# Kernel optimization log

Hardware: AMD Instinct MI355X
Metric: run time of the kernel (lower is better)

Reference implementation:

```python
import jax, jax.numpy as jnp
import numpy as np

THRESH = 0.5
MARGIN = 0.1
SCALE_POS = 2.0
SCALE_NEG = 40.0
EPS = 1e-5


def setup_inputs() -> dict:
    key = jax.random.key(0)
    k1, k2 = jax.random.split(key)
    B, D, C = 8192, 512, 512
    feats = jax.random.normal(k1, (B, D), dtype=jnp.float32)
    labels = jax.random.randint(k2, (B,), 0, C, dtype=jnp.int32)
    return {"feats": feats, "labels": labels}


def reference(feats, labels):
    B = feats.shape[0]
    inv_b = 1.0 / B
    # L2-normalize rows, cosine similarity matrix [B, B]
    f = feats / jnp.linalg.norm(feats, axis=1, keepdims=True)
    sim = f @ f.T

    same = labels[:, None] == labels[None, :]
    # positive pairs: same label AND sim < 1 - eps (excludes self-similarity)
    pos_mask = same & (sim < 1.0 - EPS)
    neg_mask = ~same

    pos_cnt = jnp.sum(pos_mask, axis=1)
    neg_cnt = jnp.sum(neg_mask, axis=1)
    valid1 = (pos_cnt >= 1) & (neg_cnt >= 1)  # row contributes to avg_ap/avg_an

    pos_sum_sim = jnp.sum(jnp.where(pos_mask, sim, 0.0), axis=1)
    neg_sum_sim = jnp.sum(jnp.where(neg_mask, sim, 0.0), axis=1)
    mean_pos = pos_sum_sim / jnp.maximum(pos_cnt, 1)
    mean_neg = neg_sum_sim / jnp.maximum(neg_cnt, 1)

    min_pos = jnp.min(jnp.where(pos_mask, sim, jnp.inf), axis=1)
    max_neg = jnp.max(jnp.where(neg_mask, sim, -jnp.inf), axis=1)

    # hard mining: neg_pair + margin > min(pos), pos_pair - margin < max(neg)
    neg_sel = neg_mask & (sim + MARGIN > min_pos[:, None])
    pos_sel = pos_mask & (sim - MARGIN < max_neg[:, None])
    valid2 = (jnp.sum(pos_sel, axis=1) >= 1) & (jnp.sum(neg_sel, axis=1) >= 1)
    valid = valid1 & valid2

    pos_exp = jnp.sum(jnp.where(pos_sel, jnp.exp(-SCALE_POS * (sim - THRESH)), 0.0), axis=1)
    neg_exp = jnp.sum(jnp.where(neg_sel, jnp.exp(SCALE_NEG * (sim - THRESH)), 0.0), axis=1)
    row_loss = (1.0 / SCALE_POS) * jnp.log1p(pos_exp) + (1.0 / SCALE_NEG) * jnp.log1p(neg_exp)

    loss = jnp.sum(jnp.where(valid, row_loss, 0.0)) * inv_b
    avg_ap = jnp.sum(jnp.where(valid1, mean_pos, 0.0)) * inv_b
    avg_an = jnp.sum(jnp.where(valid1, mean_neg, 0.0)) * inv_b
    return (loss.reshape(-1), avg_ap, avg_an)
```

## Files before the change

### kernel.cpp

```cpp
#include <hip/hip_runtime.h>
#include <math.h>

typedef float floatx4 __attribute__((ext_vector_type(4)));
typedef short short8 __attribute__((ext_vector_type(8)));
typedef unsigned short ushort4v __attribute__((ext_vector_type(4)));
typedef unsigned short ushort8v __attribute__((ext_vector_type(8)));

#define MARGIN_ 0.1f
#define THRESH_ 0.5f

__device__ __forceinline__ unsigned short f2bf(float f){
  unsigned int x = __float_as_uint(f);
  x += 0x7FFFu + ((x >> 16) & 1u);
  return (unsigned short)(x >> 16);
}
__device__ __forceinline__ float bf2f(unsigned short u){
  return __uint_as_float(((unsigned int)u) << 16);
}

__device__ __forceinline__ void gld16(const unsigned short* g, unsigned short* l){
  __builtin_amdgcn_global_load_lds(
      (const __attribute__((address_space(1))) unsigned int*)(g),
      (__attribute__((address_space(3))) unsigned int*)(l), 16, 0, 0);
}

__global__ __launch_bounds__(64) void k_norm(const float* __restrict__ feats,
                                             unsigned short* __restrict__ fbf){
  const int row = blockIdx.x;
  const int l = threadIdx.x;
  const float* rp = feats + (size_t)row * 512;
  float4 v0 = ((const float4*)rp)[2 * l];
  float4 v1 = ((const float4*)rp)[2 * l + 1];
  float ss = v0.x*v0.x + v0.y*v0.y + v0.z*v0.z + v0.w*v0.w
           + v1.x*v1.x + v1.y*v1.y + v1.z*v1.z + v1.w*v1.w;
  #pragma unroll
  for(int m = 1; m < 64; m <<= 1) ss += __shfl_xor(ss, m);
  const float rn = 1.0f / sqrtf(ss);
  short8 pk;
  pk[0] = (short)f2bf(v0.x*rn); pk[1] = (short)f2bf(v0.y*rn);
  pk[2] = (short)f2bf(v0.z*rn); pk[3] = (short)f2bf(v0.w*rn);
  pk[4] = (short)f2bf(v1.x*rn); pk[5] = (short)f2bf(v1.y*rn);
  pk[6] = (short)f2bf(v1.z*rn); pk[7] = (short)f2bf(v1.w*rn);
  ((short8*)(fbf + (size_t)row * 512))[l] = pk;
}

__global__ __launch_bounds__(256) void k_hist(const int* __restrict__ labels, int Bn,
                                              int* __restrict__ cnt){
  __shared__ int h[512];
  for(int i = threadIdx.x; i < 512; i += 256) h[i] = 0;
  __syncthreads();
  for(int i = threadIdx.x; i < Bn; i += 256) atomicAdd(&h[labels[i]], 1);
  __syncthreads();
  for(int i = threadIdx.x; i < 512; i += 256) cnt[i] = h[i];
}

__global__ __launch_bounds__(256) void k_perm(const int* __restrict__ labels,
                                              unsigned short* __restrict__ labp, int Bn){
  const int i = blockIdx.x * 256 + threadIdx.x;
  if(i < Bn) labp[i] = (unsigned short)labels[(i & ~63) + ((i & 3) * 16) + ((i >> 2) & 15)];
}

__global__ __launch_bounds__(256) void k_gemm_sym(const unsigned short* __restrict__ fbf,
                                                  unsigned short* __restrict__ simb,
                                                  int Bn){
  const int bx = blockIdx.x, by = blockIdx.y;
  if(by > bx) return;
  const bool diag = (by == bx);

  __shared__ __align__(16) unsigned short Ald[128 * 32];
  __shared__ __align__(16) unsigned short Bld[128 * 32];

  const int t = threadIdx.x;
  const int lane = t & 63, wave = t >> 6;
  const int wm = wave >> 1, wn = wave & 1;
  const int lc = lane & 15, lk = lane >> 4;
  const int row0 = by * 128, col0 = bx * 128;

  floatx4 acc[4][4];
  #pragma unroll
  for(int i = 0; i < 4; i++)
    #pragma unroll
    for(int j = 0; j < 4; j++) acc[i][j] = (floatx4){0.f, 0.f, 0.f, 0.f};

  const int rsub  = lane >> 2;
  const int slotg = (lane & 3) ^ ((lane >> 3) & 3);
  const unsigned short* gA0 = fbf + (size_t)(row0 + wave*32 + rsub) * 512 + slotg * 8;
  const unsigned short* gB0 = fbf + (size_t)(col0 + wave*32 + rsub) * 512 + slotg * 8;
  unsigned short* lA0 = Ald + wave * 1024;
  unsigned short* lB0 = Bld + wave * 1024;
  const int kswz = lk ^ ((lc >> 1) & 3);

  for(int k0 = 0; k0 < 512; k0 += 32){
    __syncthreads();
    gld16(gA0 + k0,            lA0);
    gld16(gA0 + 16*512 + k0,   lA0 + 512);
    gld16(gB0 + k0,            lB0);
    gld16(gB0 + 16*512 + k0,   lB0 + 512);
    __syncthreads();
    short8 av[4], bv[4];
    #pragma unroll
    for(int mi = 0; mi < 4; mi++) av[mi] = ((const short8*)Ald)[(wm*64 + mi*16 + lc)*4 + kswz];
    #pragma unroll
    for(int ni = 0; ni < 4; ni++) bv[ni] = ((const short8*)Bld)[(wn*64 + ni*16 + lc)*4 + kswz];
    #pragma unroll
    for(int mi = 0; mi < 4; mi++)
      #pragma unroll
      for(int ni = 0; ni < 4; ni++)
        acc[mi][ni] = __builtin_amdgcn_mfma_f32_16x16x32_bf16(av[mi], bv[ni], acc[mi][ni], 0, 0, 0);
  }

  unsigned short b[4][4][4];
  #pragma unroll
  for(int mi = 0; mi < 4; mi++)
    #pragma unroll
    for(int ni = 0; ni < 4; ni++)
      #pragma unroll
      for(int r = 0; r < 4; r++) b[mi][ni][r] = f2bf(acc[mi][ni][r]);

  #pragma unroll
  for(int mi = 0; mi < 4; mi++){
    #pragma unroll
    for(int r = 0; r < 4; r++){
      const int row = row0 + wm*64 + mi*16 + lk*4 + r;
      ushort4v v;
      v[0] = b[mi][0][r]; v[1] = b[mi][1][r]; v[2] = b[mi][2][r]; v[3] = b[mi][3][r];
      *(ushort4v*)(simb + (size_t)row * Bn + col0 + wn*64 + lc*4) = v;
    }
  }

  if(!diag){
    #pragma unroll
    for(int ni = 0; ni < 4; ni++){
      const size_t crow = (size_t)(col0 + wn*64 + ni*16 + lc) * Bn;
      #pragma unroll
      for(int r = 0; r < 4; r++){
        ushort4v v;
        v[0] = b[0][ni][r]; v[1] = b[1][ni][r]; v[2] = b[2][ni][r]; v[3] = b[3][ni][r];
        *(ushort4v*)(simb + crow + row0 + wm*64 + 16*lk + 4*r) = v;
      }
    }
  }
}

template<int NPT>
__global__ __launch_bounds__(256) void k_fused(const unsigned short* __restrict__ simb,
                                               const int* __restrict__ labels,
                                               const unsigned short* __restrict__ labp,
                                               const int* __restrict__ cnt,
                                               float* __restrict__ rl,
                                               float* __restrict__ apv,
                                               float* __restrict__ anv, int Bn){
  const int row = blockIdx.x;
  const int t = threadIdx.x, lane = t & 63, wave = t >> 6;
  const unsigned short* srow = simb + (size_t)row * Bn;
  const int labi = labels[row];
  const int a = row & 63;
  const int selfpos = (row & ~63) + ((a & 15) * 4) + (a >> 4);

  __shared__ float rq0[4], rq1[4], rq2[4], rq3[4];
  __shared__ int fl[2];
  if(t < 2) fl[t] = 0;

  ushort8v sv[NPT];
  unsigned int pmask[NPT], nmask[NPT];

  float ps = 0.f, tot = 0.f, mn = INFINITY, mx = -INFINITY;
  #pragma unroll
  for(int c = 0; c < NPT; c++){
    const int idx = c * 256 + t;
    sv[c] = ((const ushort8v*)srow)[idx];
    const ushort8v lb = ((const ushort8v*)labp)[idx];
    const int j0 = idx * 8;
    const unsigned int selfm =
        ((unsigned int)(selfpos - j0) < 8u) ? (1u << (selfpos - j0)) : 0u;
    unsigned int sm = 0;
    #pragma unroll
    for(int e = 0; e < 8; e++) sm |= (((int)lb[e] == labi) ? 1u : 0u) << e;
    const unsigned int pm = sm & ~selfm;
    pmask[c] = pm;
    nmask[c] = (~sm) & 0xFFu;
    #pragma unroll
    for(int e = 0; e < 8; e++){
      const float s = bf2f(sv[c][e]);
      tot += s;
      const bool p = (pm >> e) & 1u;
      const bool n = (nmask[c] >> e) & 1u;
      ps += p ? s : 0.f;
      mn = p ? fminf(mn, s) : mn;
      mx = n ? fmaxf(mx, s) : mx;
    }
    if(selfm) tot -= bf2f(sv[c][selfpos - j0]);
  }
  #pragma unroll
  for(int m = 1; m < 64; m <<= 1){
    ps += __shfl_xor(ps, m); tot += __shfl_xor(tot, m);
    mn = fminf(mn, __shfl_xor(mn, m)); mx = fmaxf(mx, __shfl_xor(mx, m));
  }
  if(lane == 0){ rq0[wave] = ps; rq1[wave] = tot; rq2[wave] = mn; rq3[wave] = mx; }
  __syncthreads();
  const float bps    = rq0[0] + rq0[1] + rq0[2] + rq0[3];
  const float btot   = rq1[0] + rq1[1] + rq1[2] + rq1[3];
  const float minpos = fminf(fminf(rq2[0], rq2[1]), fminf(rq2[2], rq2[3]));
  const float maxneg = fmaxf(fmaxf(rq3[0], rq3[1]), fmaxf(rq3[2], rq3[3]));
  __syncthreads();

  float pe = 0.f, ne = 0.f;
  bool pA = false, nA = false;
  #pragma unroll
  for(int c = 0; c < NPT; c++){
    #pragma unroll
    for(int e = 0; e < 8; e++){
      const float s = bf2f(sv[c][e]);
      const bool psel = ((pmask[c] >> e) & 1u) && (s - MARGIN_ < maxneg);
      const bool nsel = ((nmask[c] >> e) & 1u) && (s + MARGIN_ > minpos);
      const float arg = psel ? (THRESH_ - s) * 2.0f : (s - THRESH_) * 40.0f;
      const float ex = __expf(arg);
      pe += psel ? ex : 0.f;
      ne += nsel ? ex : 0.f;
      pA = pA || psel;
      nA = nA || nsel;
    }
  }
  const unsigned long long bp = __ballot((int)pA);
  const unsigned long long bn = __ballot((int)nA);
  #pragma unroll
  for(int m = 1; m < 64; m <<= 1){
    pe += __shfl_xor(pe, m); ne += __shfl_xor(ne, m);
  }
  if(lane == 0){
    rq0[wave] = pe; rq1[wave] = ne;
    if(bp) fl[0] = 1;
    if(bn) fl[1] = 1;
  }
  __syncthreads();
  if(t == 0){
    const float spe = rq0[0] + rq0[1] + rq0[2] + rq0[3];
    const float sne = rq1[0] + rq1[1] + rq1[2] + rq1[3];
    const int c = cnt[labi];
    const float pc = (float)(c - 1);
    const float nc = (float)(Bn - c);
    const bool v1 = (pc >= 1.f) && (nc >= 1.f);
    const bool valid = v1 && (fl[0] != 0) && (fl[1] != 0);
    rl[row]  = valid ? (0.5f * log1pf(spe) + 0.025f * log1pf(sne)) : 0.f;
    apv[row] = v1 ? bps / fmaxf(pc, 1.f) : 0.f;
    anv[row] = v1 ? (btot - bps) / fmaxf(nc, 1.f) : 0.f;
  }
}

__global__ __launch_bounds__(256) void k_fused_gen(const unsigned short* __restrict__ simb,
                                                   const int* __restrict__ labels,
                                                   const unsigned short* __restrict__ labp,
                                                   const int* __restrict__ cnt,
                                                   float* __restrict__ rl,
                                                   float* __restrict__ apv,
                                                   float* __restrict__ anv, int Bn){
  const int row = blockIdx.x;
  const int t = threadIdx.x, lane = t & 63, wave = t >> 6;
  const unsigned short* srow = simb + (size_t)row * Bn;
  const int labi = labels[row];
  const int a = row & 63;
  const int selfpos = (row & ~63) + ((a & 15) * 4) + (a >> 4);
  const int npt = Bn >> 11;

  __shared__ float rq0[4], rq1[4], rq2[4], rq3[4];
  __shared__ int fl[2];
  if(t < 2) fl[t] = 0;

  float ps = 0.f, tot = 0.f, mn = INFINITY, mx = -INFINITY;
  for(int c2 = 0; c2 < npt; c2++){
    const int idx = c2 * 256 + t;
    const ushort8v svv = ((const ushort8v*)srow)[idx];
    const ushort8v lb = ((const ushort8v*)labp)[idx];
    const int j0 = idx * 8;
    #pragma unroll
    for(int e = 0; e < 8; e++){
      const float s = bf2f(svv[e]);
      const bool same = ((int)lb[e] == labi);
      const bool self = ((j0 + e) == selfpos);
      if(!self) tot += s;
      if(same && !self){ ps += s; mn = fminf(mn, s); }
      if(!same) mx = fmaxf(mx, s);
    }
  }
  #pragma unroll
  for(int m = 1; m < 64; m <<= 1){
    ps += __shfl_xor(ps, m); tot += __shfl_xor(tot, m);
    mn = fminf(mn, __shfl_xor(mn, m)); mx = fmaxf(mx, __shfl_xor(mx, m));
  }
  if(lane == 0){ rq0[wave] = ps; rq1[wave] = tot; rq2[wave] = mn; rq3[wave] = mx; }
  __syncthreads();
  const float bps    = rq0[0] + rq0[1] + rq0[2] + rq0[3];
  const float btot   = rq1[0] + rq1[1] + rq1[2] + rq1[3];
  const float minpos = fminf(fminf(rq2[0], rq2[1]), fminf(rq2[2], rq2[3]));
  const float maxneg = fmaxf(fmaxf(rq3[0], rq3[1]), fmaxf(rq3[2], rq3[3]));
  __syncthreads();

  float pe = 0.f, ne = 0.f;
  bool pA = false, nA = false;
  for(int c2 = 0; c2 < npt; c2++){
    const int idx = c2 * 256 + t;
    const ushort8v svv = ((const ushort8v*)srow)[idx];
    const ushort8v lb = ((const ushort8v*)labp)[idx];
    const int j0 = idx * 8;
    #pragma unroll
    for(int e = 0; e < 8; e++){
      const float s = bf2f(svv[e]);
      const bool same = ((int)lb[e] == labi);
      const bool self = ((j0 + e) == selfpos);
      const bool psel = same && !self && (s - MARGIN_ < maxneg);
      const bool nsel = (!same) && (s + MARGIN_ > minpos);
      const float arg = psel ? (THRESH_ - s) * 2.0f : (s - THRESH_) * 40.0f;
      const float ex = __expf(arg);
      pe += psel ? ex : 0.f;
      ne += nsel ? ex : 0.f;
      pA = pA || psel;
      nA = nA || nsel;
    }
  }
  const unsigned long long bp = __ballot((int)pA);
  const unsigned long long bn = __ballot((int)nA);
  #pragma unroll
  for(int m = 1; m < 64; m <<= 1){
    pe += __shfl_xor(pe, m); ne += __shfl_xor(ne, m);
  }
  if(lane == 0){
    rq0[wave] = pe; rq1[wave] = ne;
    if(bp) fl[0] = 1;
    if(bn) fl[1] = 1;
  }
  __syncthreads();
  if(t == 0){
    const float spe = rq0[0] + rq0[1] + rq0[2] + rq0[3];
    const float sne = rq1[0] + rq1[1] + rq1[2] + rq1[3];
    const int c = cnt[labi];
    const float pc = (float)(c - 1);
    const float nc = (float)(Bn - c);
    const bool v1 = (pc >= 1.f) && (nc >= 1.f);
    const bool valid = v1 && (fl[0] != 0) && (fl[1] != 0);
    rl[row]  = valid ? (0.5f * log1pf(spe) + 0.025f * log1pf(sne)) : 0.f;
    apv[row] = v1 ? bps / fmaxf(pc, 1.f) : 0.f;
    anv[row] = v1 ? (btot - bps) / fmaxf(nc, 1.f) : 0.f;
  }
}

__global__ __launch_bounds__(256) void k_sum(const float* __restrict__ rl,
                                             const float* __restrict__ apv,
                                             const float* __restrict__ anv,
                                             float* __restrict__ blk, int Bn){
  const int t = threadIdx.x;
  const int row = blockIdx.x * 256 + t;
  float r = rl[row], a1 = apv[row], a2 = anv[row];
  #pragma unroll
  for(int off = 32; off; off >>= 1){
    r += __shfl_down(r, off); a1 += __shfl_down(a1, off); a2 += __shfl_down(a2, off);
  }
  __shared__ float red[3][4];
  const int lane = t & 63, wave = t >> 6;
  if(lane == 0){ red[0][wave] = r; red[1][wave] = a1; red[2][wave] = a2; }
  __syncthreads();
  if(t == 0){
    blk[blockIdx.x*3 + 0] = red[0][0] + red[0][1] + red[0][2] + red[0][3];
    blk[blockIdx.x*3 + 1] = red[1][0] + red[1][1] + red[1][2] + red[1][3];
    blk[blockIdx.x*3 + 2] = red[2][0] + red[2][1] + red[2][2] + red[2][3];
  }
}

__global__ void k_final(const float* __restrict__ blk, int nblk, float inv_b,
                        float* __restrict__ out){
  if(threadIdx.x == 0 && blockIdx.x == 0){
    float l = 0, a = 0, n = 0;
    for(int i = 0; i < nblk; i++){ l += blk[i*3]; a += blk[i*3 + 1]; n += blk[i*3 + 2]; }
    out[0] = l * inv_b;
    out[1] = a * inv_b;
    out[2] = n * inv_b;
  }
}

__global__ __launch_bounds__(256) void k_pass1(const unsigned short* __restrict__ fbf,
                                               const int* __restrict__ labels,
                                               float* __restrict__ part,
                                               int Bn, int ncb){
  __shared__ __align__(16) unsigned short Ald[128 * 32];
  __shared__ __align__(16) unsigned short Bld[128 * 32];
  __shared__ int Lrow[128], Lcol[128];
  __shared__ float Sps[2][128], Stot[2][128], Smin[2][128], Smax[2][128];

  const int t = threadIdx.x;
  const int lane = t & 63, wave = t >> 6;
  const int wm = wave >> 1, wn = wave & 1;
  const int lc = lane & 15, lk = lane >> 4;
  const int row0 = blockIdx.y * 128, col0 = blockIdx.x * 128;

  if(t < 128){
    Lrow[t] = labels[row0 + t];
    Lcol[t] = labels[col0 + t];
  }

  floatx4 acc[4][4];
  #pragma unroll
  for(int i = 0; i < 4; i++)
    #pragma unroll
    for(int j = 0; j < 4; j++) acc[i][j] = (floatx4){0.f, 0.f, 0.f, 0.f};

  const int rsub  = lane >> 2;
  const int slotg = (lane & 3) ^ ((lane >> 3) & 3);
  const unsigned short* gA0 = fbf + (size_t)(row0 + wave*32 + rsub) * 512 + slotg * 8;
  const unsigned short* gB0 = fbf + (size_t)(col0 + wave*32 + rsub) * 512 + slotg * 8;
  unsigned short* lA0 = Ald + wave * 1024;
  unsigned short* lB0 = Bld + wave * 1024;
  const int kswz = lk ^ ((lc >> 1) & 3);

  for(int k0 = 0; k0 < 512; k0 += 32){
    __syncthreads();
    gld16(gA0 + k0,            lA0);
    gld16(gA0 + 16*512 + k0,   lA0 + 512);
    gld16(gB0 + k0,            lB0);
    gld16(gB0 + 16*512 + k0,   lB0 + 512);
    __syncthreads();
    short8 av[4], bv[4];
    #pragma unroll
    for(int mi = 0; mi < 4; mi++) av[mi] = ((const short8*)Ald)[(wm*64 + mi*16 + lc)*4 + kswz];
    #pragma unroll
    for(int ni = 0; ni < 4; ni++) bv[ni] = ((const short8*)Bld)[(wn*64 + ni*16 + lc)*4 + kswz];
    #pragma unroll
    for(int mi = 0; mi < 4; mi++)
      #pragma unroll
      for(int ni = 0; ni < 4; ni++)
        acc[mi][ni] = __builtin_amdgcn_mfma_f32_16x16x32_bf16(av[mi], bv[ni], acc[mi][ni], 0, 0, 0);
  }

  int labj[4], gj[4];
  #pragma unroll
  for(int ni = 0; ni < 4; ni++){
    const int cl = wn*64 + ni*16 + lc;
    labj[ni] = Lcol[cl]; gj[ni] = col0 + cl;
  }
  #pragma unroll
  for(int mi = 0; mi < 4; mi++){
    #pragma unroll
    for(int r = 0; r < 4; r++){
      const int rowl = wm*64 + mi*16 + lk*4 + r;
      const int labi = Lrow[rowl];
      const int gi = row0 + rowl;
      float ps = 0.f, tot = 0.f, mn = INFINITY, mx = -INFINITY;
      #pragma unroll
      for(int ni = 0; ni < 4; ni++){
        const float s = acc[mi][ni][r];
        const bool same = (labi == labj[ni]);
        const bool self = (gi == gj[ni]);
        if(!self) tot += s;
        if(same && !self){ ps += s; mn = fminf(mn, s); }
        if(!same) mx = fmaxf(mx, s);
      }
      #pragma unroll
      for(int m = 1; m < 16; m <<= 1){
        ps += __shfl_xor(ps, m); tot += __shfl_xor(tot, m);
        mn = fminf(mn, __shfl_xor(mn, m)); mx = fmaxf(mx, __shfl_xor(mx, m));
      }
      if(lc == 0){
        Sps[wn][rowl] = ps; Stot[wn][rowl] = tot;
        Smin[wn][rowl] = mn; Smax[wn][rowl] = mx;
      }
    }
  }
  __syncthreads();
  if(t < 128){
    const size_t stride = (size_t)ncb * Bn;
    const size_t base = (size_t)blockIdx.x * Bn + row0 + t;
    part[0*stride + base] = Sps[0][t] + Sps[1][t];
    part[1*stride + base] = Stot[0][t] + Stot[1][t];
    part[2*stride + base] = fminf(Smin[0][t], Smin[1][t]);
    part[3*stride + base] = fmaxf(Smax[0][t], Smax[1][t]);
  }
}

__global__ __launch_bounds__(256) void k_reduce1(const float* __restrict__ part,
                                                 const int* __restrict__ labels,
                                                 const int* __restrict__ cnt,
                                                 float* __restrict__ st,
                                                 int Bn, int ncb){
  const int row = blockIdx.x * 256 + threadIdx.x;
  if(row >= Bn) return;
  const size_t stride = (size_t)ncb * Bn;
  float ps = 0, tot = 0, mn = INFINITY, mx = -INFINITY;
  for(int cb = 0; cb < ncb; cb++){
    const size_t base = (size_t)cb * Bn + row;
    ps  += part[0*stride + base];
    tot += part[1*stride + base];
    mn = fminf(mn, part[2*stride + base]);
    mx = fmaxf(mx, part[3*stride + base]);
  }
  const int c = cnt[labels[row]];
  const float pc = (float)(c - 1);
  const float nc = (float)(Bn - c);
  st[0*Bn + row] = mn;
  st[1*Bn + row] = mx;
  st[2*Bn + row] = ps / fmaxf(pc, 1.f);
  st[3*Bn + row] = (tot - ps) / fmaxf(nc, 1.f);
  st[4*Bn + row] = (pc >= 1.f && nc >= 1.f) ? 1.f : 0.f;
}

__global__ __launch_bounds__(256) void k_pass2(const unsigned short* __restrict__ fbf,
                                               const int* __restrict__ labels,
                                               const float* __restrict__ st,
                                               float* __restrict__ part,
                                               int Bn, int ncb){
  __shared__ __align__(16) unsigned short Ald[128 * 32];
  __shared__ __align__(16) unsigned short Bld[128 * 32];
  __shared__ int Lrow[128], Lcol[128];
  __shared__ float Minp[128], Maxn[128];
  __shared__ float Spe[2][128], Sne[2][128], Spf[2][128], Snf[2][128];

  const int t = threadIdx.x;
  const int lane = t & 63, wave = t >> 6;
  const int wm = wave >> 1, wn = wave & 1;
  const int lc = lane & 15, lk = lane >> 4;
  const int row0 = blockIdx.y * 128, col0 = blockIdx.x * 128;

  if(t < 128){
    Lrow[t] = labels[row0 + t];
    Lcol[t] = labels[col0 + t];
    Minp[t] = st[0*Bn + row0 + t];
    Maxn[t] = st[1*Bn + row0 + t];
  }

  floatx4 acc[4][4];
  #pragma unroll
  for(int i = 0; i < 4; i++)
    #pragma unroll
    for(int j = 0; j < 4; j++) acc[i][j] = (floatx4){0.f, 0.f, 0.f, 0.f};

  const int rsub  = lane >> 2;
  const int slotg = (lane & 3) ^ ((lane >> 3) & 3);
  const unsigned short* gA0 = fbf + (size_t)(row0 + wave*32 + rsub) * 512 + slotg * 8;
  const unsigned short* gB0 = fbf + (size_t)(col0 + wave*32 + rsub) * 512 + slotg * 8;
  unsigned short* lA0 = Ald + wave * 1024;
  unsigned short* lB0 = Bld + wave * 1024;
  const int kswz = lk ^ ((lc >> 1) & 3);

  for(int k0 = 0; k0 < 512; k0 += 32){
    __syncthreads();
    gld16(gA0 + k0,            lA0);
    gld16(gA0 + 16*512 + k0,   lA0 + 512);
    gld16(gB0 + k0,            lB0);
    gld16(gB0 + 16*512 + k0,   lB0 + 512);
    __syncthreads();
    short8 av[4], bv[4];
    #pragma unroll
    for(int mi = 0; mi < 4; mi++) av[mi] = ((const short8*)Ald)[(wm*64 + mi*16 + lc)*4 + kswz];
    #pragma unroll
    for(int ni = 0; ni < 4; ni++) bv[ni] = ((const short8*)Bld)[(wn*64 + ni*16 + lc)*4 + kswz];
    #pragma unroll
    for(int mi = 0; mi < 4; mi++)
      #pragma unroll
      for(int ni = 0; ni < 4; ni++)
        acc[mi][ni] = __builtin_amdgcn_mfma_f32_16x16x32_bf16(av[mi], bv[ni], acc[mi][ni], 0, 0, 0);
  }

  int labj[4], gj[4];
  #pragma unroll
  for(int ni = 0; ni < 4; ni++){
    const int cl = wn*64 + ni*16 + lc;
    labj[ni] = Lcol[cl]; gj[ni] = col0 + cl;
  }
  #pragma unroll
  for(int mi = 0; mi < 4; mi++){
    #pragma unroll
    for(int r = 0; r < 4; r++){
      const int rowl = wm*64 + mi*16 + lk*4 + r;
      const int labi = Lrow[rowl];
      const int gi = row0 + rowl;
      const float mp  = Minp[rowl];
      const float mxn = Maxn[rowl];
      float pe = 0.f, ne = 0.f;
      bool pa = false, na = false;
      #pragma unroll
      for(int ni = 0; ni < 4; ni++){
        const float s = acc[mi][ni][r];
        const bool same = (labi == labj[ni]);
        const bool self = (gi == gj[ni]);
        if(same && !self && (s - MARGIN_ < mxn)){
          pe += __expf(-2.0f * (s - THRESH_)); pa = true;
        }
        if(!same && (s + MARGIN_ > mp)){
          ne += __expf(40.0f * (s - THRESH_)); na = true;
        }
      }
      const unsigned long long bp  = __ballot((int)pa);
      const unsigned long long bn2 = __ballot((int)na);
      #pragma unroll
      for(int m = 1; m < 16; m <<= 1){
        pe += __shfl_xor(pe, m); ne += __shfl_xor(ne, m);
      }
      if(lc == 0){
        Spe[wn][rowl] = pe; Sne[wn][rowl] = ne;
        Spf[wn][rowl] = ((bp  >> (lk*16)) & 0xFFFFull) ? 1.f : 0.f;
        Snf[wn][rowl] = ((bn2 >> (lk*16)) & 0xFFFFull) ? 1.f : 0.f;
      }
    }
  }
  __syncthreads();
  if(t < 128){
    const size_t stride = (size_t)ncb * Bn;
    const size_t base = (size_t)blockIdx.x * Bn + row0 + t;
    part[0*stride + base] = Spe[0][t] + Spe[1][t];
    part[1*stride + base] = Sne[0][t] + Sne[1][t];
    part[2*stride + base] = fmaxf(Spf[0][t], Spf[1][t]);
    part[3*stride + base] = fmaxf(Snf[0][t], Snf[1][t]);
  }
}

__global__ __launch_bounds__(256) void k_reduce2f(const float* __restrict__ part,
                                                  const float* __restrict__ st,
                                                  float* __restrict__ rowloss,
                                                  float* __restrict__ apv,
                                                  float* __restrict__ anv,
                                                  int Bn, int ncb){
  const int row = blockIdx.x * 256 + threadIdx.x;
  if(row >= Bn) return;
  const size_t stride = (size_t)ncb * Bn;
  float pe = 0, ne = 0, pf = 0, nf = 0;
  for(int cb = 0; cb < ncb; cb++){
    const size_t base = (size_t)cb * Bn + row;
    pe += part[0*stride + base]; ne += part[1*stride + base];
    pf = fmaxf(pf, part[2*stride + base]); nf = fmaxf(nf, part[3*stride + base]);
  }
  const float v1 = st[4*Bn + row];
  const bool valid = (v1 > 0.5f) && (pf > 0.5f) && (nf > 0.5f);
  rowloss[row] = valid ? (0.5f * log1pf(pe) + 0.025f * log1pf(ne)) : 0.f;
  apv[row] = (v1 > 0.5f) ? st[2*Bn + row] : 0.f;
  anv[row] = (v1 > 0.5f) ? st[3*Bn + row] : 0.f;
}

extern "C" void kernel_launch(void* const* d_in, const int* in_sizes, int n_in,
                              void* d_out, int out_size, void* d_ws, size_t ws_size,
                              hipStream_t stream){
  const float* feats = (const float*)d_in[0];
  const int* labels = (const int*)d_in[1];
  float* out = (float*)d_out;
  const int Bn  = in_sizes[1];
  const int ncb = Bn / 128;

  char* ws = (char*)d_ws;
  size_t off = 0;
  unsigned short* fbf = (unsigned short*)(ws + off); off += (size_t)Bn * 512 * 2;
  float* part = (float*)(ws + off); off += (size_t)4 * ncb * Bn * 4;
  float* st   = (float*)(ws + off); off += (size_t)5 * Bn * 4;
  int*   cnt  = (int*)(ws + off);   off += 4096;
  unsigned short* labp = (unsigned short*)(ws + off); off += (size_t)Bn * 2;
  off = (off + 255) & ~(size_t)255;
  float* rl   = (float*)(ws + off); off += (size_t)Bn * 4;
  float* apv  = (float*)(ws + off); off += (size_t)Bn * 4;
  float* anv  = (float*)(ws + off); off += (size_t)Bn * 4;
  float* blk  = (float*)(ws + off); off += 4096;
  off = (off + 255) & ~(size_t)255;
  unsigned short* simb = (unsigned short*)(ws + off);
  const size_t need = off + (size_t)Bn * Bn * 2;
  const bool mat = (ws_size >= need);

  k_norm<<<Bn, 64, 0, stream>>>(feats, fbf);
  k_hist<<<1, 256, 0, stream>>>(labels, Bn, cnt);
  if(mat){
    k_perm<<<(Bn + 255) / 256, 256, 0, stream>>>(labels, labp, Bn);
    dim3 g(Bn / 128, Bn / 128);
    k_gemm_sym<<<g, 256, 0, stream>>>(fbf, simb, Bn);
    if(Bn == 8192){
      k_fused<4><<<Bn, 256, 0, stream>>>(simb, labels, labp, cnt, rl, apv, anv, Bn);
    } else {
      k_fused_gen<<<Bn, 256, 0, stream>>>(simb, labels, labp, cnt, rl, apv, anv, Bn);
    }
  } else {
    dim3 g(ncb, Bn / 128);
    k_pass1<<<g, 256, 0, stream>>>(fbf, labels, part, Bn, ncb);
    k_reduce1<<<Bn / 256, 256, 0, stream>>>(part, labels, cnt, st, Bn, ncb);
    k_pass2<<<g, 256, 0, stream>>>(fbf, labels, st, part, Bn, ncb);
    k_reduce2f<<<Bn / 256, 256, 0, stream>>>(part, st, rl, apv, anv, Bn, ncb);
  }
  k_sum<<<Bn / 256, 256, 0, stream>>>(rl, apv, anv, blk, Bn);
  k_final<<<1, 64, 0, stream>>>(blk, Bn / 256, 1.0f / (float)Bn, out);
}
```

Measured before the change: 155.5 us.

## Compact GEMM grid to triangle tiles, merge hist/perm, batch rows per block

Launches the symmetric GEMM over only the upper-triangle tile list, decoding each linear block index to a (row, col) tile with a sqrt estimate and an XCD-aware interleave. This removes the empty lower-triangle blocks. The transposed tile writeback now uses 16-byte stores instead of 8-byte ones. The label histogram and permutation kernels are merged into one grid-wide kernel using global atomics after a memset, and the fused row kernel now handles four rows per block to cut the block count. The trade-offs are extra index math per GEMM block, global atomic contention on the counts, and less parallelism in the row kernel.

```diff
diff --git a/kernel.cpp b/kernel.cpp
--- a/kernel.cpp
+++ b/kernel.cpp
@@ -44,27 +44,30 @@
   ((short8*)(fbf + (size_t)row * 512))[l] = pk;
 }
 
-__global__ __launch_bounds__(256) void k_hist(const int* __restrict__ labels, int Bn,
-                                              int* __restrict__ cnt){
-  __shared__ int h[512];
-  for(int i = threadIdx.x; i < 512; i += 256) h[i] = 0;
-  __syncthreads();
-  for(int i = threadIdx.x; i < Bn; i += 256) atomicAdd(&h[labels[i]], 1);
-  __syncthreads();
-  for(int i = threadIdx.x; i < 512; i += 256) cnt[i] = h[i];
-}
-
-__global__ __launch_bounds__(256) void k_perm(const int* __restrict__ labels,
-                                              unsigned short* __restrict__ labp, int Bn){
+__global__ __launch_bounds__(256) void k_prep(const int* __restrict__ labels,
+                                              unsigned short* __restrict__ labp,
+                                              int* __restrict__ cnt, int Bn){
   const int i = blockIdx.x * 256 + threadIdx.x;
-  if(i < Bn) labp[i] = (unsigned short)labels[(i & ~63) + ((i & 3) * 16) + ((i >> 2) & 15)];
-}
-
+  if(i < Bn){
+    labp[i] = (unsigned short)labels[(i & ~63) + ((i & 3) * 16) + ((i >> 2) & 15)];
+    atomicAdd(&cnt[labels[i]], 1);
+  }
+}
+
+#define TRI_S(y) ((y)*n - (((y)*((y)-1))>>1))
 __global__ __launch_bounds__(256) void k_gemm_sym(const unsigned short* __restrict__ fbf,
                                                   unsigned short* __restrict__ simb,
-                                                  int Bn){
-  const int bx = blockIdx.x, by = blockIdx.y;
-  if(by > bx) return;
+                                                  int Bn, int nTri){
+  const int n = Bn >> 7;
+  int i = blockIdx.x;
+  int j;
+  if((nTri & 7) == 0){ const int c = nTri >> 3; j = (i & 7) * c + (i >> 3); }
+  else j = i;
+  int by = (int)(((float)(2*n + 1) - sqrtf((float)((2*n+1)*(2*n+1) - 8*j))) * 0.5f);
+  if(by < 0) by = 0;
+  while(TRI_S(by + 1) <= j) by++;
+  while(TRI_S(by) > j) by--;
+  const int bx = by + (j - TRI_S(by));
   const bool diag = (by == bx);
 
   __shared__ __align__(16) unsigned short Ald[128 * 32];
@@ -78,9 +81,9 @@
 
   floatx4 acc[4][4];
   #pragma unroll
-  for(int i = 0; i < 4; i++)
-    #pragma unroll
-    for(int j = 0; j < 4; j++) acc[i][j] = (floatx4){0.f, 0.f, 0.f, 0.f};
+  for(int a = 0; a < 4; a++)
+    #pragma unroll
+    for(int b2 = 0; b2 < 4; b2++) acc[a][b2] = (floatx4){0.f, 0.f, 0.f, 0.f};
 
   const int rsub  = lane >> 2;
   const int slotg = (lane & 3) ^ ((lane >> 3) & 3);
@@ -133,117 +136,125 @@
     for(int ni = 0; ni < 4; ni++){
       const size_t crow = (size_t)(col0 + wn*64 + ni*16 + lc) * Bn;
       #pragma unroll
-      for(int r = 0; r < 4; r++){
-        ushort4v v;
-        v[0] = b[0][ni][r]; v[1] = b[1][ni][r]; v[2] = b[2][ni][r]; v[3] = b[3][ni][r];
-        *(ushort4v*)(simb + crow + row0 + wm*64 + 16*lk + 4*r) = v;
+      for(int h = 0; h < 2; h++){
+        ushort8v v;
+        v[0] = b[0][ni][2*h];   v[1] = b[1][ni][2*h];
+        v[2] = b[2][ni][2*h];   v[3] = b[3][ni][2*h];
+        v[4] = b[0][ni][2*h+1]; v[5] = b[1][ni][2*h+1];
+        v[6] = b[2][ni][2*h+1]; v[7] = b[3][ni][2*h+1];
+        *(ushort8v*)(simb + crow + row0 + wm*64 + 16*lk + 8*h) = v;
       }
     }
   }
 }
 
 template<int NPT>
-__global__ __launch_bounds__(256) void k_fused(const unsigned short* __restrict__ simb,
-                                               const int* __restrict__ labels,
-                                               const unsigned short* __restrict__ labp,
-                                               const int* __restrict__ cnt,
-                                               float* __restrict__ rl,
-                                               float* __restrict__ apv,
-                                               float* __restrict__ anv, int Bn){
-  const int row = blockIdx.x;
+__global__ __launch_bounds__(256) void k_fused4(const unsigned short* __restrict__ simb,
+                                                const int* __restrict__ labels,
+                                                const unsigned short* __restrict__ labp,
+                                                const int* __restrict__ cnt,
+                                                float* __restrict__ rl,
+                                                float* __restrict__ apv,
+                                                float* __restrict__ anv, int Bn){
   const int t = threadIdx.x, lane = t & 63, wave = t >> 6;
-  const unsigned short* srow = simb + (size_t)row * Bn;
-  const int labi = labels[row];
-  const int a = row & 63;
-  const int selfpos = (row & ~63) + ((a & 15) * 4) + (a >> 4);
-
   __shared__ float rq0[4], rq1[4], rq2[4], rq3[4];
   __shared__ int fl[2];
-  if(t < 2) fl[t] = 0;
-
-  ushort8v sv[NPT];
-  unsigned int pmask[NPT], nmask[NPT];
-
-  float ps = 0.f, tot = 0.f, mn = INFINITY, mx = -INFINITY;
-  #pragma unroll
-  for(int c = 0; c < NPT; c++){
-    const int idx = c * 256 + t;
-    sv[c] = ((const ushort8v*)srow)[idx];
-    const ushort8v lb = ((const ushort8v*)labp)[idx];
-    const int j0 = idx * 8;
-    const unsigned int selfm =
-        ((unsigned int)(selfpos - j0) < 8u) ? (1u << (selfpos - j0)) : 0u;
-    unsigned int sm = 0;
-    #pragma unroll
-    for(int e = 0; e < 8; e++) sm |= (((int)lb[e] == labi) ? 1u : 0u) << e;
-    const unsigned int pm = sm & ~selfm;
-    pmask[c] = pm;
-    nmask[c] = (~sm) & 0xFFu;
-    #pragma unroll
-    for(int e = 0; e < 8; e++){
-      const float s = bf2f(sv[c][e]);
-      tot += s;
-      const bool p = (pm >> e) & 1u;
-      const bool n = (nmask[c] >> e) & 1u;
-      ps += p ? s : 0.f;
-      mn = p ? fminf(mn, s) : mn;
-      mx = n ? fmaxf(mx, s) : mx;
-    }
-    if(selfm) tot -= bf2f(sv[c][selfpos - j0]);
-  }
-  #pragma unroll
-  for(int m = 1; m < 64; m <<= 1){
-    ps += __shfl_xor(ps, m); tot += __shfl_xor(tot, m);
-    mn = fminf(mn, __shfl_xor(mn, m)); mx = fmaxf(mx, __shfl_xor(mx, m));
-  }
-  if(lane == 0){ rq0[wave] = ps; rq1[wave] = tot; rq2[wave] = mn; rq3[wave] = mx; }
-  __syncthreads();
-  const float bps    = rq0[0] + rq0[1] + rq0[2] + rq0[3];
-  const float btot   = rq1[0] + rq1[1] + rq1[2] + rq1[3];
-  const float minpos = fminf(fminf(rq2[0], rq2[1]), fminf(rq2[2], rq2[3]));
-  const float maxneg = fmaxf(fmaxf(rq3[0], rq3[1]), fmaxf(rq3[2], rq3[3]));
-  __syncthreads();
-
-  float pe = 0.f, ne = 0.f;
-  bool pA = false, nA = false;
-  #pragma unroll
-  for(int c = 0; c < NPT; c++){
-    #pragma unroll
-    for(int e = 0; e < 8; e++){
-      const float s = bf2f(sv[c][e]);
-      const bool psel = ((pmask[c] >> e) & 1u) && (s - MARGIN_ < maxneg);
-      const bool nsel = ((nmask[c] >> e) & 1u) && (s + MARGIN_ > minpos);
-      const float arg = psel ? (THRESH_ - s) * 2.0f : (s - THRESH_) * 40.0f;
-      const float ex = __expf(arg);
-      pe += psel ? ex : 0.f;
-      ne += nsel ? ex : 0.f;
-      pA = pA || psel;
-      nA = nA || nsel;
-    }
-  }
-  const unsigned long long bp = __ballot((int)pA);
-  const unsigned long long bn = __ballot((int)nA);
-  #pragma unroll
-  for(int m = 1; m < 64; m <<= 1){
-    pe += __shfl_xor(pe, m); ne += __shfl_xor(ne, m);
-  }
-  if(lane == 0){
-    rq0[wave] = pe; rq1[wave] = ne;
-    if(bp) fl[0] = 1;
-    if(bn) fl[1] = 1;
-  }
-  __syncthreads();
-  if(t == 0){
-    const float spe = rq0[0] + rq0[1] + rq0[2] + rq0[3];
-    const float sne = rq1[0] + rq1[1] + rq1[2] + rq1[3];
-    const int c = cnt[labi];
-    const float pc = (float)(c - 1);
-    const float nc = (float)(Bn - c);
-    const bool v1 = (pc >= 1.f) && (nc >= 1.f);
-    const bool valid = v1 && (fl[0] != 0) && (fl[1] != 0);
-    rl[row]  = valid ? (0.5f * log1pf(spe) + 0.025f * log1pf(sne)) : 0.f;
-    apv[row] = v1 ? bps / fmaxf(pc, 1.f) : 0.f;
-    anv[row] = v1 ? (btot - bps) / fmaxf(nc, 1.f) : 0.f;
+
+  for(int rr = 0; rr < 4; rr++){
+    const int row = blockIdx.x * 4 + rr;
+    __syncthreads();
+    if(t < 2) fl[t] = 0;
+    __syncthreads();
+
+    const unsigned short* srow = simb + (size_t)row * Bn;
+    const int labi = labels[row];
+    const int a = row & 63;
+    const int selfpos = (row & ~63) + ((a & 15) * 4) + (a >> 4);
+
+    ushort8v sv[NPT];
+    unsigned int pmask[NPT], nmask[NPT];
+
+    float ps = 0.f, tot = 0.f, mn = INFINITY, mx = -INFINITY;
+    #pragma unroll
+    for(int c = 0; c < NPT; c++){
+      const int idx = c * 256 + t;
+      sv[c] = ((const ushort8v*)srow)[idx];
+      const ushort8v lb = ((const ushort8v*)labp)[idx];
+      const int j0 = idx * 8;
+      const unsigned int selfm =
+          ((unsigned int)(selfpos - j0) < 8u) ? (1u << (selfpos - j0)) : 0u;
+      unsigned int sm = 0;
+      #pragma unroll
+      for(int e = 0; e < 8; e++) sm |= (((int)lb[e] == labi) ? 1u : 0u) << e;
+      const unsigned int pm = sm & ~selfm;
+      pmask[c] = pm;
+      nmask[c] = (~sm) & 0xFFu;
+      #pragma unroll
+      for(int e = 0; e < 8; e++){
+        const float s = bf2f(sv[c][e]);
+        tot += s;
+        const bool p = (pm >> e) & 1u;
+        const bool nn = (nmask[c] >> e) & 1u;
+        ps += p ? s : 0.f;
+        mn = p ? fminf(mn, s) : mn;
+        mx = nn ? fmaxf(mx, s) : mx;
+      }
+      if(selfm) tot -= bf2f(sv[c][selfpos - j0]);
+    }
+    #pragma unroll
+    for(int m = 1; m < 64; m <<= 1){
+      ps += __shfl_xor(ps, m); tot += __shfl_xor(tot, m);
+      mn = fminf(mn, __shfl_xor(mn, m)); mx = fmaxf(mx, __shfl_xor(mx, m));
+    }
+    if(lane == 0){ rq0[wave] = ps; rq1[wave] = tot; rq2[wave] = mn; rq3[wave] = mx; }
+    __syncthreads();
+    const float bps    = rq0[0] + rq0[1] + rq0[2] + rq0[3];
+    const float btot   = rq1[0] + rq1[1] + rq1[2] + rq1[3];
+    const float minpos = fminf(fminf(rq2[0], rq2[1]), fminf(rq2[2], rq2[3]));
+    const float maxneg = fmaxf(fmaxf(rq3[0], rq3[1]), fmaxf(rq3[2], rq3[3]));
+    __syncthreads();
+
+    float pe = 0.f, ne = 0.f;
+    bool pA = false, nA = false;
+    #pragma unroll
+    for(int c = 0; c < NPT; c++){
+      #pragma unroll
+      for(int e = 0; e < 8; e++){
+        const float s = bf2f(sv[c][e]);
+        const bool psel = ((pmask[c] >> e) & 1u) && (s - MARGIN_ < maxneg);
+        const bool nsel = ((nmask[c] >> e) & 1u) && (s + MARGIN_ > minpos);
+        const float arg = psel ? (THRESH_ - s) * 2.0f : (s - THRESH_) * 40.0f;
+        const float ex = __expf(arg);
+        pe += psel ? ex : 0.f;
+        ne += nsel ? ex : 0.f;
+        pA = pA || psel;
+        nA = nA || nsel;
+      }
+    }
+    const unsigned long long bp = __ballot((int)pA);
+    const unsigned long long bn = __ballot((int)nA);
+    #pragma unroll
+    for(int m = 1; m < 64; m <<= 1){
+      pe += __shfl_xor(pe, m); ne += __shfl_xor(ne, m);
+    }
+    if(lane == 0){
+      rq0[wave] = pe; rq1[wave] = ne;
+      if(bp) fl[0] = 1;
+      if(bn) fl[1] = 1;
+    }
+    __syncthreads();
+    if(t == 0){
+      const float spe = rq0[0] + rq0[1] + rq0[2] + rq0[3];
+      const float sne = rq1[0] + rq1[1] + rq1[2] + rq1[3];
+      const int c = cnt[labi];
+      const float pc = (float)(c - 1);
+      const float nc = (float)(Bn - c);
+      const bool v1 = (pc >= 1.f) && (nc >= 1.f);
+      const bool valid = v1 && (fl[0] != 0) && (fl[1] != 0);
+      rl[row]  = valid ? (0.5f * log1pf(spe) + 0.025f * log1pf(sne)) : 0.f;
+      apv[row] = v1 ? bps / fmaxf(pc, 1.f) : 0.f;
+      anv[row] = v1 ? (btot - bps) / fmaxf(nc, 1.f) : 0.f;
+    }
   }
 }
 
@@ -640,6 +651,7 @@
   float* out = (float*)d_out;
   const int Bn  = in_sizes[1];
   const int ncb = Bn / 128;
+  const int nTri = ncb * (ncb + 1) / 2;
 
   char* ws = (char*)d_ws;
   size_t off = 0;
@@ -658,14 +670,13 @@
   const size_t need = off + (size_t)Bn * Bn * 2;
   const bool mat = (ws_size >= need);
 
+  hipMemsetAsync(cnt, 0, 512 * sizeof(int), stream);
   k_norm<<<Bn, 64, 0, stream>>>(feats, fbf);
-  k_hist<<<1, 256, 0, stream>>>(labels, Bn, cnt);
+  k_prep<<<(Bn + 255) / 256, 256, 0, stream>>>(labels, labp, cnt, Bn);
   if(mat){
-    k_perm<<<(Bn + 255) / 256, 256, 0, stream>>>(labels, labp, Bn);
-    dim3 g(Bn / 128, Bn / 128);
-    k_gemm_sym<<<g, 256, 0, stream>>>(fbf, simb, Bn);
+    k_gemm_sym<<<nTri, 256, 0, stream>>>(fbf, simb, Bn, nTri);
     if(Bn == 8192){
-      k_fused<4><<<Bn, 256, 0, stream>>>(simb, labels, labp, cnt, rl, apv, anv, Bn);
+      k_fused4<4><<<Bn / 4, 256, 0, stream>>>(simb, labels, labp, cnt, rl, apv, anv, Bn);
     } else {
       k_fused_gen<<<Bn, 256, 0, stream>>>(simb, labels, labp, cnt, rl, apv, anv, Bn);
     }
```

New measurement: 161.6 us. 4.0% more time.
